# Performance work log

Hardware: AMD Instinct MI355X
Metric: run time of the kernel (lower is better)

The kernel has to match this reference:

```python
import jax, jax.numpy as jnp
from jax import lax
import numpy as np


def setup_inputs() -> dict:
    key = jax.random.key(0)
    k1, k2 = jax.random.split(key)
    B, T, C = 32, 8192, 3   # batch, series length, channels
    NS, LS = 256, 32        # num shapelets, shapelet length
    data = jax.random.normal(k1, (B, T, C), dtype=jnp.float32)
    kernel = jax.random.normal(k2, (NS, LS, C), dtype=jnp.float32)
    return {"data": data, "kernel": kernel}


def reference(data, kernel):
    """Shapelet transform: min over sliding windows of mean squared distance.

    data:   [B, T, C]
    kernel: [NS, LS, C] (shapelets)
    out:    [B, NS]  = min_w sum_{l,c} (data[b, w+l, c] - kernel[s, l, c])^2 / LS
    Uses the convolution identity ||a - k||^2 = ||a||^2 + ||k||^2 - 2 a.k to
    avoid materializing the [NS, B, W, LS, C] broadcast of the TF original.
    """
    B, T, C = data.shape
    NS, LS, _ = kernel.shape
    W = T - LS + 1  # number of valid windows

    # cross[b, s, w] = sum_{l,c} data[b, w+l, c] * kernel[s, l, c] via 1D conv
    cross = lax.conv_general_dilated(
        data.transpose(0, 2, 1),          # [B, C, T]
        kernel.transpose(0, 2, 1),        # [NS, C, LS]
        window_strides=(1,), padding="VALID",
        dimension_numbers=("NCH", "OIH", "NCH"))  # -> [B, NS, W]

    # sliding-window squared norms of data via cumulative sums
    d2 = jnp.sum(data * data, axis=-1)                      # [B, T]
    cs = jnp.concatenate([jnp.zeros((B, 1), d2.dtype),
                          jnp.cumsum(d2, axis=1)], axis=1)  # [B, T+1]
    a2 = cs[:, LS:] - cs[:, :-LS]                           # [B, W]

    k2 = jnp.sum(kernel * kernel, axis=(1, 2))              # [NS]

    dist = a2[:, None, :] + k2[None, :, None] - 2.0 * cross  # [B, NS, W]
    out = jnp.min(dist, axis=-1) / LS                        # [B, NS]
    return out
```

## Files before the change

### kernel.cpp

```cpp
#include <hip/hip_runtime.h>
#include <hip/hip_bf16.h>

#define BB 32
#define TT 8192
#define CC 3
#define NSS 256
#define LSS 32
#define JL (LSS * CC)
#define WW (TT - LSS + 1)
#define WTILE 512
#define NWTILE (TT / WTILE)
#define NE (WTILE * CC + JL - CC)
#define NPK (NE - 1)
#define NP 1793
#define NTHREADS 256
#define PER_T 7
#define INFBITS 0x7F800000

typedef __attribute__((ext_vector_type(8))) short bf16x8;
typedef __attribute__((ext_vector_type(16))) float f32x16;
typedef __attribute__((ext_vector_type(4))) unsigned int uint4v;

__device__ __forceinline__ unsigned int bf16pk(float a, float b) {
  unsigned ua = __float_as_uint(a), ub = __float_as_uint(b);
  ua = (ua + 0x7FFFu + ((ua >> 16) & 1u)) >> 16;
  ub = (ub + 0x7FFFu + ((ub >> 16) & 1u)) >> 16;
  return ua | (ub << 16);
}

__device__ __forceinline__ bf16x8 mk8(unsigned u0, unsigned u1, unsigned u2, unsigned u3) {
  uint4v u = {u0, u1, u2, u3};
  return __builtin_bit_cast(bf16x8, u);
}

__global__ __launch_bounds__(NTHREADS) void init_out_kernel(float* out, int n) {
  int i = blockIdx.x * blockDim.x + threadIdx.x;
  if (i < n) out[i] = __int_as_float(INFBITS);
}

__global__ __launch_bounds__(NTHREADS, 2) void shapelet_mfma_kernel(
    const float* __restrict__ data, const float* __restrict__ kern,
    float* __restrict__ out) {
  __shared__ unsigned int spk[NPK];
  __shared__ float p[NP];
  __shared__ float a2[WTILE];
  __shared__ float k2arr[NSS];
  __shared__ float wsum[4];
  __shared__ float fin[4][4][32];

  const int tid  = threadIdx.x;
  const int lane = tid & 63;
  const int wave = tid >> 6;
  const int wn = wave & 1;
  const int wm = wave >> 1;
  const int wt = blockIdx.x;
  const int b  = blockIdx.y;
  const int t0 = wt * WTILE;
  const long ebase = (long)b * (TT * CC) + (long)t0 * CC;
  const int evalid = (TT - t0) * CC;

  float e[PER_T + 1], sq[PER_T];
  float part = 0.f;
  const int i0 = tid * PER_T;
  #pragma unroll
  for (int r = 0; r < PER_T + 1; ++r) {
    const int i = i0 + r;
    float v = 0.f;
    if (i < NE && i < evalid) v = data[ebase + i];
    e[r] = v;
  }
  #pragma unroll
  for (int r = 0; r < PER_T; ++r) { sq[r] = e[r] * e[r]; part += sq[r]; }
  #pragma unroll
  for (int r = 0; r < PER_T; ++r) {
    const int i = i0 + r;
    if (i < NPK) spk[i] = bf16pk(e[r], e[r + 1]);
  }

  float incl = part;
  #pragma unroll
  for (int m = 1; m < 64; m <<= 1) {
    float o = __shfl_up(incl, m, 64);
    if (lane >= m) incl += o;
  }
  if (lane == 63) wsum[wave] = incl;

  {
    const float* kp = kern + tid * JL;
    float acc = 0.f;
    #pragma unroll
    for (int j = 0; j < JL; j += 4) {
      float4 v = *reinterpret_cast<const float4*>(kp + j);
      acc = fmaf(v.x, v.x, fmaf(v.y, v.y, fmaf(v.z, v.z, fmaf(v.w, v.w, acc))));
    }
    k2arr[tid] = acc;
  }
  __syncthreads();

  {
    float woff = 0.f;
    for (int wv = 0; wv < wave; ++wv) woff += wsum[wv];
    float run = woff + (incl - part);
    #pragma unroll
    for (int r = 0; r < PER_T; ++r) { p[i0 + r] = run; run += sq[r]; }
  }

  bf16x8 bfr[6][4];
  {
    const int col = lane & 31, g = lane >> 5;
    #pragma unroll
    for (int ks = 0; ks < 6; ++ks) {
      #pragma unroll
      for (int nf = 0; nf < 4; ++nf) {
        const int s = wn * 128 + nf * 32 + col;
        const float* kp = kern + s * JL + ks * 16 + g * 8;
        float4 x = *reinterpret_cast<const float4*>(kp);
        float4 y = *reinterpret_cast<const float4*>(kp + 4);
        bfr[ks][nf] = mk8(bf16pk(x.x, x.y), bf16pk(x.z, x.w),
                          bf16pk(y.x, y.y), bf16pk(y.z, y.w));
      }
    }
  }
  __syncthreads();

  for (int w = tid; w < WTILE; w += NTHREADS) {
    const int gw = t0 + w;
    a2[w] = (gw < WW) ? (p[3 * w + JL] - p[3 * w]) : __int_as_float(INFBITS);
  }
  __syncthreads();

  const int mrow = lane & 31, hi = lane >> 5;
  const int lb = 3 * mrow + 8 * hi;
  const float INF = __int_as_float(INFBITS);
  float runmin[4] = {INF, INF, INF, INF};
  f32x16 z16 = {0.f};

  for (int mt = wm; mt < WTILE / 32; mt += 2) {
    const int q0 = mt * JL + lb;
    bf16x8 af[6];
    #pragma unroll
    for (int ks = 0; ks < 6; ++ks) {
      const int q = q0 + ks * 16;
      af[ks] = mk8(spk[q], spk[q + 2], spk[q + 4], spk[q + 6]);
    }
    f32x16 acc[4];
    #pragma unroll
    for (int nf = 0; nf < 4; ++nf)
      acc[nf] = __builtin_amdgcn_mfma_f32_32x32x16_bf16(af[0], bfr[0][nf], z16, 0, 0, 0);
    #pragma unroll
    for (int ks = 1; ks < 6; ++ks) {
      #pragma unroll
      for (int nf = 0; nf < 4; ++nf)
        acc[nf] = __builtin_amdgcn_mfma_f32_32x32x16_bf16(af[ks], bfr[ks][nf], acc[nf], 0, 0, 0);
    }
    float a2r[16];
    #pragma unroll
    for (int r = 0; r < 16; ++r)
      a2r[r] = a2[mt * 32 + (r & 3) + 8 * (r >> 2) + 4 * hi];
    #pragma unroll
    for (int nf = 0; nf < 4; ++nf) {
      #pragma unroll
      for (int r = 0; r < 16; ++r)
        runmin[nf] = fminf(runmin[nf], fmaf(-2.f, acc[nf][r], a2r[r]));
    }
  }

  #pragma unroll
  for (int nf = 0; nf < 4; ++nf) {
    float v = runmin[nf];
    v = fminf(v, __shfl_xor(v, 32, 64));
    if (lane < 32) fin[wave][nf][lane] = v;
  }
  __syncthreads();

  {
    const int wn_o = tid >> 7, nf_o = (tid >> 5) & 3, col = tid & 31;
    const float v = fminf(fin[wn_o][nf_o][col], fin[wn_o + 2][nf_o][col]);
    const int s = wn_o * 128 + nf_o * 32 + col;
    const float res = (v + k2arr[s]) * (1.0f / 32.0f);
    atomicMin((int*)out + ((long)b * NSS + s), __float_as_int(res));
  }
}

extern "C" void kernel_launch(void* const* d_in, const int* in_sizes, int n_in,
                              void* d_out, int out_size, void* d_ws, size_t ws_size,
                              hipStream_t stream) {
  const float* data = (const float*)d_in[0];
  const float* kern = (const float*)d_in[1];
  float* out = (float*)d_out;

  hipLaunchKernelGGL(init_out_kernel, dim3((BB * NSS + NTHREADS - 1) / NTHREADS),
                     dim3(NTHREADS), 0, stream, out, BB * NSS);

  dim3 grid(NWTILE, BB);
  hipLaunchKernelGGL(shapelet_mfma_kernel, grid, dim3(NTHREADS), 0, stream,
                     data, kern, out);
}
```

Baseline: 80.22 us.

## Split preprocessing into prep kernel writing packed bf16 data and norms to workspace

New measurement: 76.91 us. 4.1% less time.

```diff
diff --git a/kernel.cpp b/kernel.cpp
--- a/kernel.cpp
+++ b/kernel.cpp
@@ -10,16 +10,16 @@
 #define WW (TT - LSS + 1)
 #define WTILE 512
 #define NWTILE (TT / WTILE)
-#define NE (WTILE * CC + JL - CC)
-#define NPK (NE - 1)
-#define NP 1793
+#define ROWW (TT * CC)
+#define NE2 1629
+#define NPK2 1628
+#define SPK_ROWS 33
 #define NTHREADS 256
-#define PER_T 7
 #define INFBITS 0x7F800000
+#define NEGINFBITS 0xFF800000
 
 typedef __attribute__((ext_vector_type(8))) short bf16x8;
 typedef __attribute__((ext_vector_type(16))) float f32x16;
-typedef __attribute__((ext_vector_type(4))) unsigned int uint4v;
 
 __device__ __forceinline__ unsigned int bf16pk(float a, float b) {
   unsigned ua = __float_as_uint(a), ub = __float_as_uint(b);
@@ -29,112 +29,113 @@
 }
 
 __device__ __forceinline__ bf16x8 mk8(unsigned u0, unsigned u1, unsigned u2, unsigned u3) {
-  uint4v u = {u0, u1, u2, u3};
-  return __builtin_bit_cast(bf16x8, u);
-}
-
-__global__ __launch_bounds__(NTHREADS) void init_out_kernel(float* out, int n) {
-  int i = blockIdx.x * blockDim.x + threadIdx.x;
-  if (i < n) out[i] = __int_as_float(INFBITS);
-}
-
-__global__ __launch_bounds__(NTHREADS, 2) void shapelet_mfma_kernel(
-    const float* __restrict__ data, const float* __restrict__ kern,
+  union { unsigned u[4]; bf16x8 v; } c;
+  c.u[0] = u0; c.u[1] = u1; c.u[2] = u2; c.u[3] = u3;
+  return c.v;
+}
+
+__global__ __launch_bounds__(NTHREADS) void prep_kernel(
+    const float* __restrict__ data, const float* __restrict__ kernm,
+    unsigned int* __restrict__ spk_g, float* __restrict__ a2_g,
+    uint4* __restrict__ kpk_g, float* __restrict__ k2_g,
     float* __restrict__ out) {
-  __shared__ unsigned int spk[NPK];
-  __shared__ float p[NP];
-  __shared__ float a2[WTILE];
-  __shared__ float k2arr[NSS];
-  __shared__ float wsum[4];
-  __shared__ float fin[4][4][32];
-
-  const int tid  = threadIdx.x;
-  const int lane = tid & 63;
-  const int wave = tid >> 6;
-  const int wn = wave & 1;
-  const int wm = wave >> 1;
-  const int wt = blockIdx.x;
-  const int b  = blockIdx.y;
-  const int t0 = wt * WTILE;
-  const long ebase = (long)b * (TT * CC) + (long)t0 * CC;
-  const int evalid = (TT - t0) * CC;
-
-  float e[PER_T + 1], sq[PER_T];
-  float part = 0.f;
-  const int i0 = tid * PER_T;
-  #pragma unroll
-  for (int r = 0; r < PER_T + 1; ++r) {
-    const int i = i0 + r;
-    float v = 0.f;
-    if (i < NE && i < evalid) v = data[ebase + i];
-    e[r] = v;
-  }
-  #pragma unroll
-  for (int r = 0; r < PER_T; ++r) { sq[r] = e[r] * e[r]; part += sq[r]; }
-  #pragma unroll
-  for (int r = 0; r < PER_T; ++r) {
-    const int i = i0 + r;
-    if (i < NPK) spk[i] = bf16pk(e[r], e[r + 1]);
-  }
-
-  float incl = part;
-  #pragma unroll
-  for (int m = 1; m < 64; m <<= 1) {
-    float o = __shfl_up(incl, m, 64);
-    if (lane >= m) incl += o;
-  }
-  if (lane == 63) wsum[wave] = incl;
-
-  {
-    const float* kp = kern + tid * JL;
+  const int tid = threadIdx.x;
+  const int x = blockIdx.x, b = blockIdx.y;
+
+  if (x == NWTILE) {
+    if (b != 0) return;
+    const int s = tid;
+    const float* kp = kernm + s * JL;
+    float f[JL];
     float acc = 0.f;
     #pragma unroll
     for (int j = 0; j < JL; j += 4) {
       float4 v = *reinterpret_cast<const float4*>(kp + j);
+      f[j] = v.x; f[j + 1] = v.y; f[j + 2] = v.z; f[j + 3] = v.w;
       acc = fmaf(v.x, v.x, fmaf(v.y, v.y, fmaf(v.z, v.z, fmaf(v.w, v.w, acc))));
     }
-    k2arr[tid] = acc;
-  }
-  __syncthreads();
-
-  {
-    float woff = 0.f;
-    for (int wv = 0; wv < wave; ++wv) woff += wsum[wv];
-    float run = woff + (incl - part);
-    #pragma unroll
-    for (int r = 0; r < PER_T; ++r) { p[i0 + r] = run; run += sq[r]; }
-  }
-
-  bf16x8 bfr[6][4];
-  {
-    const int col = lane & 31, g = lane >> 5;
+    k2_g[s] = acc;
+    const int wn = s >> 7, nf = (s >> 5) & 3, col = s & 31;
     #pragma unroll
     for (int ks = 0; ks < 6; ++ks) {
       #pragma unroll
-      for (int nf = 0; nf < 4; ++nf) {
-        const int s = wn * 128 + nf * 32 + col;
-        const float* kp = kern + s * JL + ks * 16 + g * 8;
-        float4 x = *reinterpret_cast<const float4*>(kp);
-        float4 y = *reinterpret_cast<const float4*>(kp + 4);
-        bfr[ks][nf] = mk8(bf16pk(x.x, x.y), bf16pk(x.z, x.w),
-                          bf16pk(y.x, y.y), bf16pk(y.z, y.w));
+      for (int g = 0; g < 2; ++g) {
+        const float* q = f + ks * 16 + g * 8;
+        uint4 u;
+        u.x = bf16pk(q[0], q[1]); u.y = bf16pk(q[2], q[3]);
+        u.z = bf16pk(q[4], q[5]); u.w = bf16pk(q[6], q[7]);
+        kpk_g[((wn * 6 + ks) * 4 + nf) * 64 + g * 32 + col] = u;
       }
     }
+    for (int i = tid; i < BB * NSS; i += NTHREADS)
+      out[i] = __int_as_float(INFBITS);
+    return;
+  }
+
+  __shared__ float e[NE2];
+  const int t0 = x * WTILE;
+  const int base = 3 * t0;
+  const float* drow = data + (size_t)b * ROWW;
+  for (int i = tid; i < NE2; i += NTHREADS) {
+    const int gi = base + i;
+    e[i] = (gi < ROWW) ? drow[gi] : 0.f;
   }
   __syncthreads();
 
-  for (int w = tid; w < WTILE; w += NTHREADS) {
-    const int gw = t0 + w;
-    a2[w] = (gw < WW) ? (p[3 * w + JL] - p[3 * w]) : __int_as_float(INFBITS);
-  }
+  unsigned int* srow = spk_g + (size_t)b * ROWW;
+  for (int i = tid; i < NPK2; i += NTHREADS) {
+    const int j = base + i;
+    if (j < ROWW - 1) srow[j] = bf16pk(e[i], e[i + 1]);
+  }
+  float* arow = a2_g + (size_t)b * TT;
+  for (int wl = tid; wl < WTILE; wl += NTHREADS) {
+    const int gw = t0 + wl;
+    if (gw < WW) {
+      float sum = 0.f;
+      for (int j = 0; j < JL; ++j) { const float v = e[3 * wl + j]; sum = fmaf(v, v, sum); }
+      arow[gw] = sum;
+    } else {
+      arow[gw] = __int_as_float(INFBITS);
+    }
+  }
+}
+
+__global__ __launch_bounds__(NTHREADS, 2) void shapelet_main(
+    const unsigned int* __restrict__ spk_g, const float* __restrict__ a2_g,
+    const uint4* __restrict__ kpk_g, const float* __restrict__ k2_g,
+    float* __restrict__ out) {
+  __shared__ unsigned int spk[NPK2];
+  __shared__ float ha2[WTILE];
+  __shared__ float fin[4][4][32];
+
+  const int tid = threadIdx.x, lane = tid & 63, wave = tid >> 6;
+  const int wn = wave & 1, wm = wave >> 1;
+  const int wt = blockIdx.x, b = blockIdx.y;
+  const int t0 = wt * WTILE;
+
+  bf16x8 bfr[6][4];
+  #pragma unroll
+  for (int ks = 0; ks < 6; ++ks) {
+    #pragma unroll
+    for (int nf = 0; nf < 4; ++nf) {
+      const uint4 u = kpk_g[((wn * 6 + ks) * 4 + nf) * 64 + lane];
+      bfr[ks][nf] = mk8(u.x, u.y, u.z, u.w);
+    }
+  }
+
+  const unsigned int* srow = spk_g + (size_t)b * ROWW + 3 * t0;
+  for (int i = tid; i < NPK2; i += NTHREADS) spk[i] = srow[i];
+  const float* arow = a2_g + (size_t)b * TT + t0;
+  ha2[tid] = arow[tid];
+  ha2[tid + NTHREADS] = arow[tid + NTHREADS];
   __syncthreads();
 
   const int mrow = lane & 31, hi = lane >> 5;
   const int lb = 3 * mrow + 8 * hi;
-  const float INF = __int_as_float(INFBITS);
-  float runmin[4] = {INF, INF, INF, INF};
-  f32x16 z16 = {0.f};
-
+  const float NEGINF = __int_as_float(NEGINFBITS);
+  float runmax[4] = {NEGINF, NEGINF, NEGINF, NEGINF};
+
+  #pragma unroll 1
   for (int mt = wm; mt < WTILE / 32; mt += 2) {
     const int q0 = mt * JL + lb;
     bf16x8 af[6];
@@ -143,6 +144,7 @@
       const int q = q0 + ks * 16;
       af[ks] = mk8(spk[q], spk[q + 2], spk[q + 4], spk[q + 6]);
     }
+    f32x16 z16 = {0.f};
     f32x16 acc[4];
     #pragma unroll
     for (int nf = 0; nf < 4; ++nf)
@@ -153,32 +155,36 @@
       for (int nf = 0; nf < 4; ++nf)
         acc[nf] = __builtin_amdgcn_mfma_f32_32x32x16_bf16(af[ks], bfr[ks][nf], acc[nf], 0, 0, 0);
     }
-    float a2r[16];
-    #pragma unroll
-    for (int r = 0; r < 16; ++r)
-      a2r[r] = a2[mt * 32 + (r & 3) + 8 * (r >> 2) + 4 * hi];
+    float4 ar[4];
+    #pragma unroll
+    for (int k = 0; k < 4; ++k)
+      ar[k] = *reinterpret_cast<const float4*>(&ha2[mt * 32 + 4 * hi + 8 * k]);
     #pragma unroll
     for (int nf = 0; nf < 4; ++nf) {
       #pragma unroll
-      for (int r = 0; r < 16; ++r)
-        runmin[nf] = fminf(runmin[nf], fmaf(-2.f, acc[nf][r], a2r[r]));
+      for (int k = 0; k < 4; ++k) {
+        const float v0 = fmaf(-0.5f, ar[k].x, acc[nf][4 * k + 0]);
+        const float v1 = fmaf(-0.5f, ar[k].y, acc[nf][4 * k + 1]);
+        const float v2 = fmaf(-0.5f, ar[k].z, acc[nf][4 * k + 2]);
+        const float v3 = fmaf(-0.5f, ar[k].w, acc[nf][4 * k + 3]);
+        runmax[nf] = fmaxf(runmax[nf], fmaxf(fmaxf(v0, v1), fmaxf(v2, v3)));
+      }
     }
   }
 
   #pragma unroll
   for (int nf = 0; nf < 4; ++nf) {
-    float v = runmin[nf];
-    v = fminf(v, __shfl_xor(v, 32, 64));
+    float v = runmax[nf];
+    v = fmaxf(v, __shfl_xor(v, 32, 64));
     if (lane < 32) fin[wave][nf][lane] = v;
   }
   __syncthreads();
 
   {
     const int wn_o = tid >> 7, nf_o = (tid >> 5) & 3, col = tid & 31;
-    const float v = fminf(fin[wn_o][nf_o][col], fin[wn_o + 2][nf_o][col]);
-    const int s = wn_o * 128 + nf_o * 32 + col;
-    const float res = (v + k2arr[s]) * (1.0f / 32.0f);
-    atomicMin((int*)out + ((long)b * NSS + s), __float_as_int(res));
+    const float M = fmaxf(fin[wn_o][nf_o][col], fin[wn_o + 2][nf_o][col]);
+    const float res = fmaf(-2.f, M, k2_g[tid]) * (1.0f / 32.0f);
+    atomicMin((int*)out + ((size_t)b * NSS + tid), __float_as_int(res));
   }
 }
 
@@ -189,10 +195,14 @@
   const float* kern = (const float*)d_in[1];
   float* out = (float*)d_out;
 
-  hipLaunchKernelGGL(init_out_kernel, dim3((BB * NSS + NTHREADS - 1) / NTHREADS),
-                     dim3(NTHREADS), 0, stream, out, BB * NSS);
-
-  dim3 grid(NWTILE, BB);
-  hipLaunchKernelGGL(shapelet_mfma_kernel, grid, dim3(NTHREADS), 0, stream,
-                     data, kern, out);
-}
+  unsigned int* spk_g = (unsigned int*)d_ws;
+  char* base = (char*)d_ws;
+  float* a2_g = (float*)(base + (size_t)SPK_ROWS * ROWW * 4);
+  uint4* kpk_g = (uint4*)(base + (size_t)SPK_ROWS * ROWW * 4 + (size_t)BB * TT * 4);
+  float* k2_g  = (float*)((char*)kpk_g + 3072 * 16);
+
+  hipLaunchKernelGGL(prep_kernel, dim3(NWTILE + 1, BB), dim3(NTHREADS), 0, stream,
+                     data, kern, spk_g, a2_g, kpk_g, k2_g, out);
+  hipLaunchKernelGGL(shapelet_main, dim3(NWTILE, BB), dim3(NTHREADS), 0, stream,
+                     spk_g, a2_g, kpk_g, k2_g, out);
+}
```
